# Kernel optimization log

Measured on AMD Instinct MI355X. Metric: run time of the kernel, lower is better.

## Reference

```python
import jax, jax.numpy as jnp
import numpy as np
from jax import lax

BN_EPS = 1e-5

def dwconv(x, w, dilation):
    # x: [N,C,H,W], w: [C,1,k,k] depthwise; SAME padding = (r*(k-1)+1)//2
    k = w.shape[-1]
    pad = (dilation * (k - 1) + 1) // 2
    return lax.conv_general_dilated(
        x, w, window_strides=(1, 1), padding=[(pad, pad), (pad, pad)],
        rhs_dilation=(dilation, dilation), feature_group_count=x.shape[1],
        dimension_numbers=('NCHW', 'OIHW', 'NCHW'))

def bn_eval(y, gamma, beta, mean, var):
    # inference BatchNorm2d over channel dim; params: [C]
    inv = gamma * lax.rsqrt(var + BN_EPS)
    return y * inv[None, :, None, None] + (beta - mean * inv)[None, :, None, None]

def setup_inputs() -> dict:
    key = jax.random.key(0)
    ks = jax.random.split(key, 13)
    C = 384
    x = jax.random.normal(ks[0], (16, C, 56, 56), jnp.float32)
    w_lk = jax.random.normal(ks[1], (C, 1, 13, 13), jnp.float32) * 0.05
    w_b0 = jax.random.normal(ks[2], (C, 1, 5, 5), jnp.float32) * 0.05
    w_b1 = jax.random.normal(ks[3], (C, 1, 7, 7), jnp.float32) * 0.05
    w_b2 = jax.random.normal(ks[4], (C, 1, 7, 7), jnp.float32) * 0.05
    w_b3 = jax.random.normal(ks[5], (C, 1, 3, 3), jnp.float32) * 0.05
    w_b4 = jax.random.normal(ks[6], (C, 1, 3, 3), jnp.float32) * 0.05
    w_b5 = jax.random.normal(ks[7], (C, 1, 3, 3), jnp.float32) * 0.05
    bn_gamma = jax.random.uniform(ks[8], (7, C), jnp.float32, 0.5, 1.5)
    bn_beta = jax.random.normal(ks[9], (7, C), jnp.float32) * 0.1
    bn_mean = jax.random.normal(ks[10], (7, C), jnp.float32) * 0.1
    bn_var = jax.random.uniform(ks[11], (7, C), jnp.float32, 0.5, 1.5)
    return dict(x=x, w_lk=w_lk, w_b0=w_b0, w_b1=w_b1, w_b2=w_b2, w_b3=w_b3,
                w_b4=w_b4, w_b5=w_b5, bn_gamma=bn_gamma, bn_beta=bn_beta,
                bn_mean=bn_mean, bn_var=bn_var)

def reference(x, w_lk, w_b0, w_b1, w_b2, w_b3, w_b4, w_b5,
              bn_gamma, bn_beta, bn_mean, bn_var):
    # DilatedReparamBlock (kernel_size=13, non-deploy):
    # out = BN(dw13(x)) + sum_i BN_i(dw_{k_i, r_i}(x))
    dilates = (1, 1, 2, 3, 4, 5)
    branch_ws = (w_b0, w_b1, w_b2, w_b3, w_b4, w_b5)
    out = bn_eval(dwconv(x, w_lk, 1), bn_gamma[0], bn_beta[0], bn_mean[0], bn_var[0])
    for i, (w, r) in enumerate(zip(branch_ws, dilates)):
        j = i + 1
        out = out + bn_eval(dwconv(x, w, r), bn_gamma[j], bn_beta[j], bn_mean[j], bn_var[j])
    return out
```

## Files before the change

### kernel.cpp

```cpp
#include <hip/hip_runtime.h>


#define CCH 384
#define SP 56
#define PW 68
#define NPLANES (16*384)
#define BLK 128

__global__ __launch_bounds__(BLK, 4) void drb_conv13_2w(
    const float* __restrict__ x,
    const float* __restrict__ w_lk, const float* __restrict__ w_b0,
    const float* __restrict__ w_b1, const float* __restrict__ w_b2,
    const float* __restrict__ w_b3, const float* __restrict__ w_b4,
    const float* __restrict__ w_b5,
    const float* __restrict__ gamma, const float* __restrict__ beta,
    const float* __restrict__ mean, const float* __restrict__ var,
    float* __restrict__ out)
{
    __shared__ __align__(16) float sx[PW * PW];
    __shared__ __align__(16) float sw[176];

    const int plane = blockIdx.x;
    const int c = plane % CCH;
    const int tid = threadIdx.x;
    const float* __restrict__ xp = x + (size_t)plane * (SP * SP);

    float S[7];
    float bias = 0.f;
    #pragma unroll
    for (int j = 0; j < 7; j++) {
        float inv = gamma[j * CCH + c] * rsqrtf(var[j * CCH + c] + 1e-5f);
        S[j] = inv;
        bias += beta[j * CCH + c] - mean[j * CCH + c] * inv;
    }

    {
        float4 z = make_float4(0.f, 0.f, 0.f, 0.f);
        #pragma unroll
        for (int k = 0; k < 10; k++) {
            int i = tid + BLK * k;
            if (i < PW * PW / 4) ((float4*)sx)[i] = z;
        }
    }
    __syncthreads();

    #pragma unroll
    for (int k = 0; k < 2; k++) {
        int t = tid + BLK * k;
        if (t < 169) {
            int ky = t / 13, kx = t - 13 * ky;
            float w = S[0] * w_lk[c * 169 + t];
            if (ky >= 4 && ky <= 8 && kx >= 4 && kx <= 8)
                w += S[1] * w_b0[c * 25 + (ky - 4) * 5 + (kx - 4)];
            if (ky >= 3 && ky <= 9 && kx >= 3 && kx <= 9)
                w += S[2] * w_b1[c * 49 + (ky - 3) * 7 + (kx - 3)];
            if (!(ky & 1) && !(kx & 1))
                w += S[3] * w_b2[c * 49 + (ky >> 1) * 7 + (kx >> 1)];
            if (ky >= 3 && ky <= 9 && (ky - 3) % 3 == 0 &&
                kx >= 3 && kx <= 9 && (kx - 3) % 3 == 0)
                w += S[4] * w_b3[c * 9 + ((ky - 3) / 3) * 3 + (kx - 3) / 3];
            if (ky >= 2 && ky <= 10 && (ky - 2) % 4 == 0 &&
                kx >= 2 && kx <= 10 && (kx - 2) % 4 == 0)
                w += S[5] * w_b4[c * 9 + ((ky - 2) / 4) * 3 + (kx - 2) / 4];
            if (ky >= 1 && ky <= 11 && (ky - 1) % 5 == 0 &&
                kx >= 1 && kx <= 11 && (kx - 1) % 5 == 0)
                w += S[6] * w_b5[c * 9 + ((ky - 1) / 5) * 3 + (kx - 1) / 5];
            sw[t] = w;
        }
    }

    #pragma unroll
    for (int k = 0; k < 7; k++) {
        int i4 = tid + BLK * k;
        if (i4 < SP * SP / 4) {
            float4 v = ((const float4*)xp)[i4];
            int r = i4 / 14;
            int col = (i4 - r * 14) * 4;
            float* d = &sx[(r + 6) * PW + col + 6];
            ((float2*)d)[0] = make_float2(v.x, v.y);
            ((float2*)d)[1] = make_float2(v.z, v.w);
        }
    }
    __syncthreads();

    const int tact = (tid < 112) ? tid : 0;
    const int xg = tact % 14;
    const int yg = tact / 14;
    const int Yb = yg * 7;
    const float* __restrict__ sbase = &sx[Yb * PW + 4 * xg];

    float acc[7][4];
    #pragma unroll
    for (int r = 0; r < 7; r++)
        #pragma unroll
        for (int j = 0; j < 4; j++) acc[r][j] = 0.f;

    #pragma unroll 1
    for (int g = 0; g < 3; g++) {
        const int k0 = g * 4;
        float4 wq[13];
        #pragma unroll
        for (int q = 0; q < 13; q++)
            wq[q] = ((const float4*)&sw[k0 * 13])[q];
        const float* w = (const float*)wq;
        const float* sr = sbase + k0 * PW;
        #pragma unroll
        for (int i = 0; i < 10; i++) {
            float4 win4[4];
            #pragma unroll
            for (int q = 0; q < 4; q++)
                win4[q] = *(const float4*)(sr + i * PW + 4 * q);
            const float* win = (const float*)win4;
            #pragma unroll
            for (int d = 0; d < 4; d++) {
                const int r = i - d;
                if (r >= 0 && r <= 6) {
                    #pragma unroll
                    for (int kx = 0; kx < 13; kx++) {
                        const float wv = w[d * 13 + kx];
                        #pragma unroll
                        for (int j = 0; j < 4; j++)
                            acc[r][j] = fmaf(wv, win[kx + j], acc[r][j]);
                    }
                }
            }
        }
    }
    {
        float wt[13];
        #pragma unroll
        for (int q = 0; q < 3; q++)
            ((float4*)wt)[q] = ((const float4*)&sw[156])[q];
        wt[12] = sw[168];
        const float* sr = sbase + 12 * PW;
        #pragma unroll
        for (int r = 0; r < 7; r++) {
            float4 win4[4];
            #pragma unroll
            for (int q = 0; q < 4; q++)
                win4[q] = *(const float4*)(sr + r * PW + 4 * q);
            const float* win = (const float*)win4;
            #pragma unroll
            for (int kx = 0; kx < 13; kx++) {
                const float wv = wt[kx];
                #pragma unroll
                for (int j = 0; j < 4; j++)
                    acc[r][j] = fmaf(wv, win[kx + j], acc[r][j]);
            }
        }
    }

    if (tid < 112) {
        float* op = out + (size_t)plane * (SP * SP) + Yb * SP + 4 * xg;
        #pragma unroll
        for (int r = 0; r < 7; r++) {
            float4 v = make_float4(acc[r][0] + bias, acc[r][1] + bias,
                                   acc[r][2] + bias, acc[r][3] + bias);
            *(float4*)(op + r * SP) = v;
        }
    }
}

extern "C" void kernel_launch(void* const* d_in, const int* in_sizes, int n_in,
                              void* d_out, int out_size, void* d_ws, size_t ws_size,
                              hipStream_t stream) {
    const float* x    = (const float*)d_in[0];
    const float* w_lk = (const float*)d_in[1];
    const float* w_b0 = (const float*)d_in[2];
    const float* w_b1 = (const float*)d_in[3];
    const float* w_b2 = (const float*)d_in[4];
    const float* w_b3 = (const float*)d_in[5];
    const float* w_b4 = (const float*)d_in[6];
    const float* w_b5 = (const float*)d_in[7];
    const float* bn_g = (const float*)d_in[8];
    const float* bn_b = (const float*)d_in[9];
    const float* bn_m = (const float*)d_in[10];
    const float* bn_v = (const float*)d_in[11];
    float* out = (float*)d_out;

    drb_conv13_2w<<<dim3(NPLANES), dim3(BLK), 0, stream>>>(
        x, w_lk, w_b0, w_b1, w_b2, w_b3, w_b4, w_b5,
        bn_g, bn_b, bn_m, bn_v, out);
}
```

Before: 252.7 us.

## Use 64-thread blocks with 7x8 register tiles and clamped zero-row padding

Each block shrinks to a single 64-thread wavefront, and each thread now computes a 7x8 output tile instead of 7x4. This widens horizontal reuse of each loaded window row and weight across more FMAs. Vertical padding rows are removed from shared memory; out-of-range rows are redirected to a single zero row, which shrinks LDS use. The cost is more accumulator registers and fewer warps per block (launch bounds 64,3), plus one idle column group of 8 threads per block (xg==7).

```diff
diff --git a/kernel.cpp b/kernel.cpp
--- a/kernel.cpp
+++ b/kernel.cpp
@@ -4,10 +4,10 @@
 #define CCH 384
 #define SP 56
 #define PW 68
+#define ZROW 56
 #define NPLANES (16*384)
-#define BLK 128
 
-__global__ __launch_bounds__(BLK, 4) void drb_conv13_2w(
+__global__ __launch_bounds__(64, 3) void drb_conv13_r5(
     const float* __restrict__ x,
     const float* __restrict__ w_lk, const float* __restrict__ w_b0,
     const float* __restrict__ w_b1, const float* __restrict__ w_b2,
@@ -17,7 +17,7 @@
     const float* __restrict__ mean, const float* __restrict__ var,
     float* __restrict__ out)
 {
-    __shared__ __align__(16) float sx[PW * PW];
+    __shared__ __align__(16) float sx[57 * PW];
     __shared__ __align__(16) float sw[176];
 
     const int plane = blockIdx.x;
@@ -37,16 +37,16 @@
     {
         float4 z = make_float4(0.f, 0.f, 0.f, 0.f);
         #pragma unroll
-        for (int k = 0; k < 10; k++) {
-            int i = tid + BLK * k;
-            if (i < PW * PW / 4) ((float4*)sx)[i] = z;
+        for (int k = 0; k < 16; k++) {
+            int i = tid + 64 * k;
+            if (i < 57 * PW / 4) ((float4*)sx)[i] = z;
         }
     }
     __syncthreads();
 
     #pragma unroll
-    for (int k = 0; k < 2; k++) {
-        int t = tid + BLK * k;
+    for (int k = 0; k < 3; k++) {
+        int t = tid + 64 * k;
         if (t < 169) {
             int ky = t / 13, kx = t - 13 * ky;
             float w = S[0] * w_lk[c * 169 + t];
@@ -70,30 +70,30 @@
     }
 
     #pragma unroll
-    for (int k = 0; k < 7; k++) {
-        int i4 = tid + BLK * k;
+    for (int k = 0; k < 13; k++) {
+        int i4 = tid + 64 * k;
         if (i4 < SP * SP / 4) {
             float4 v = ((const float4*)xp)[i4];
             int r = i4 / 14;
             int col = (i4 - r * 14) * 4;
-            float* d = &sx[(r + 6) * PW + col + 6];
+            float* d = &sx[r * PW + col + 6];
             ((float2*)d)[0] = make_float2(v.x, v.y);
             ((float2*)d)[1] = make_float2(v.z, v.w);
         }
     }
     __syncthreads();
 
-    const int tact = (tid < 112) ? tid : 0;
-    const int xg = tact % 14;
-    const int yg = tact / 14;
+    const int xg = tid & 7;
+    const int yg = tid >> 3;
+    const int xgc = (xg < 7) ? xg : 3;
     const int Yb = yg * 7;
-    const float* __restrict__ sbase = &sx[Yb * PW + 4 * xg];
+    const float* __restrict__ sbase = &sx[8 * xgc];
 
-    float acc[7][4];
+    float acc[7][8];
     #pragma unroll
     for (int r = 0; r < 7; r++)
         #pragma unroll
-        for (int j = 0; j < 4; j++) acc[r][j] = 0.f;
+        for (int j = 0; j < 8; j++) acc[r][j] = 0.f;
 
     #pragma unroll 1
     for (int g = 0; g < 3; g++) {
@@ -103,13 +103,15 @@
         for (int q = 0; q < 13; q++)
             wq[q] = ((const float4*)&sw[k0 * 13])[q];
         const float* w = (const float*)wq;
-        const float* sr = sbase + k0 * PW;
         #pragma unroll
         for (int i = 0; i < 10; i++) {
-            float4 win4[4];
+            int t = Yb + k0 + i - 6;
+            int rowidx = ((unsigned)t <= 55u) ? t : ZROW;
+            const float* sr = sbase + rowidx * PW;
+            float4 win4[5];
             #pragma unroll
-            for (int q = 0; q < 4; q++)
-                win4[q] = *(const float4*)(sr + i * PW + 4 * q);
+            for (int q = 0; q < 5; q++)
+                win4[q] = *(const float4*)(sr + 4 * q);
             const float* win = (const float*)win4;
             #pragma unroll
             for (int d = 0; d < 4; d++) {
@@ -119,7 +121,7 @@
                     for (int kx = 0; kx < 13; kx++) {
                         const float wv = w[d * 13 + kx];
                         #pragma unroll
-                        for (int j = 0; j < 4; j++)
+                        for (int j = 0; j < 8; j++)
                             acc[r][j] = fmaf(wv, win[kx + j], acc[r][j]);
                     }
                 }
@@ -132,31 +134,36 @@
         for (int q = 0; q < 3; q++)
             ((float4*)wt)[q] = ((const float4*)&sw[156])[q];
         wt[12] = sw[168];
-        const float* sr = sbase + 12 * PW;
         #pragma unroll
         for (int r = 0; r < 7; r++) {
-            float4 win4[4];
+            int t = Yb + 6 + r;
+            int rowidx = (t <= 55) ? t : ZROW;
+            const float* sr = sbase + rowidx * PW;
+            float4 win4[5];
             #pragma unroll
-            for (int q = 0; q < 4; q++)
-                win4[q] = *(const float4*)(sr + r * PW + 4 * q);
+            for (int q = 0; q < 5; q++)
+                win4[q] = *(const float4*)(sr + 4 * q);
             const float* win = (const float*)win4;
             #pragma unroll
             for (int kx = 0; kx < 13; kx++) {
                 const float wv = wt[kx];
                 #pragma unroll
-                for (int j = 0; j < 4; j++)
+                for (int j = 0; j < 8; j++)
                     acc[r][j] = fmaf(wv, win[kx + j], acc[r][j]);
             }
         }
     }
 
-    if (tid < 112) {
-        float* op = out + (size_t)plane * (SP * SP) + Yb * SP + 4 * xg;
+    if (xg < 7) {
+        float* op = out + (size_t)plane * (SP * SP) + Yb * SP + 8 * xg;
         #pragma unroll
         for (int r = 0; r < 7; r++) {
-            float4 v = make_float4(acc[r][0] + bias, acc[r][1] + bias,
-                                   acc[r][2] + bias, acc[r][3] + bias);
-            *(float4*)(op + r * SP) = v;
+            float4 v0 = make_float4(acc[r][0] + bias, acc[r][1] + bias,
+                                    acc[r][2] + bias, acc[r][3] + bias);
+            float4 v1 = make_float4(acc[r][4] + bias, acc[r][5] + bias,
+                                    acc[r][6] + bias, acc[r][7] + bias);
+            *(float4*)(op + r * SP) = v0;
+            *(float4*)(op + r * SP + 4) = v1;
         }
     }
 }
@@ -178,7 +185,7 @@
     const float* bn_v = (const float*)d_in[11];
     float* out = (float*)d_out;
 
-    drb_conv13_2w<<<dim3(NPLANES), dim3(BLK), 0, stream>>>(
+    drb_conv13_r5<<<dim3(NPLANES), dim3(64), 0, stream>>>(
         x, w_lk, w_b0, w_b1, w_b2, w_b3, w_b4, w_b5,
         bn_g, bn_b, bn_m, bn_v, out);
 }
```

Result: slower. 464.9 us (+84.0%).
